# Kernel tuning notes

Measured on AMD Instinct MI355X. Metric: run time of the kernel, lower is better.

## Reference

```python
import jax, jax.numpy as jnp
import numpy as np

INPUT_DIM = 22
H = 256            # lstm_hidden_dim
H1, H2, H3 = 1024, 512, 1024
RRI = 2
N_R = N_L = 2048
N_PAIRS = 65536


def _lstm_layer(x, Wih, Whh, bih, bhh):
    """Bidirectional LSTM layer. x: [T, D]. Wih: [2, 4H, D], Whh: [2, 4H, H],
    bih/bhh: [2, 4H]. PyTorch gate order: i, f, g, o. Returns [T, 2H]."""
    h0 = jnp.zeros((H,), x.dtype)
    c0 = jnp.zeros((H,), x.dtype)

    def run_dir(d, reverse):
        pre = x @ Wih[d].T + (bih[d] + bhh[d])  # [T, 4H] precomputed input part
        Whh_d = Whh[d]

        def step(carry, g_in):
            h, c = carry
            g = g_in + h @ Whh_d.T
            i, f, gg, o = jnp.split(g, 4)
            c = jax.nn.sigmoid(f) * c + jax.nn.sigmoid(i) * jnp.tanh(gg)
            h = jax.nn.sigmoid(o) * jnp.tanh(c)
            return (h, c), h

        _, hs = jax.lax.scan(step, (h0, c0), pre, reverse=reverse)
        return hs  # [T, H], in original time order

    return jnp.concatenate([run_dir(0, False), run_dir(1, True)], axis=-1)


def _encode(x, Wih0, Whh0, bih0, bhh0, Wih1, Whh1, bih1, bhh1,
            W1, b1, W2, b2):
    h = _lstm_layer(x, Wih0, Whh0, bih0, bhh0)      # [T, 2H]
    h = _lstm_layer(h, Wih1, Whh1, bih1, bhh1)      # [T, 2H]
    h = jax.nn.relu(h @ W1.T + b1)                  # [T, H1]
    h = jax.nn.relu(h @ W2.T + b2)                  # [T, H2]
    return h


def setup_inputs() -> dict:
    key = jax.random.key(0)
    ks = jax.random.split(key, 24)
    s = 0.05
    inp = {
        "v_r": jax.random.normal(ks[0], (N_R, INPUT_DIM), jnp.float32),
        "v_l": jax.random.normal(ks[1], (N_L, INPUT_DIM), jnp.float32),
        "pair_r": jax.random.randint(ks[2], (N_PAIRS,), 0, N_R, jnp.int32),
        "pair_l": jax.random.randint(ks[3], (N_PAIRS,), 0, N_L, jnp.int32),
        # LSTM layer 0 (input 22), layer 1 (input 2H); [dir=2, ...]
        "Wih0": jax.random.normal(ks[4], (2, 4 * H, INPUT_DIM), jnp.float32) * s,
        "Whh0": jax.random.normal(ks[5], (2, 4 * H, H), jnp.float32) * s,
        "bih0": jax.random.normal(ks[6], (2, 4 * H), jnp.float32) * s,
        "bhh0": jax.random.normal(ks[7], (2, 4 * H), jnp.float32) * s,
        "Wih1": jax.random.normal(ks[8], (2, 4 * H, 2 * H), jnp.float32) * s,
        "Whh1": jax.random.normal(ks[9], (2, 4 * H, H), jnp.float32) * s,
        "bih1": jax.random.normal(ks[10], (2, 4 * H), jnp.float32) * s,
        "bhh1": jax.random.normal(ks[11], (2, 4 * H), jnp.float32) * s,
        # MLP stacks (PyTorch Linear: y = x W^T + b)
        "W1": jax.random.normal(ks[12], (H1, 2 * H), jnp.float32) * s,
        "b1": jnp.zeros((H1,), jnp.float32),
        "W2": jax.random.normal(ks[13], (H2, H1), jnp.float32) * s,
        "b2": jnp.zeros((H2,), jnp.float32),
        "W3": jax.random.normal(ks[14], (H3, 2 * H2), jnp.float32) * s,
        "b3": jnp.zeros((H3,), jnp.float32),
        "Wout": jax.random.normal(ks[15], (RRI, H3), jnp.float32) * s,
        "bout": jnp.zeros((RRI,), jnp.float32),
    }
    return inp


def reference(v_r, v_l, pair_r, pair_l,
              Wih0, Whh0, bih0, bhh0, Wih1, Whh1, bih1, bhh1,
              W1, b1, W2, b2, W3, b3, Wout, bout):
    # Encode both chains (dropout layers act as identity in eval)
    enc_r = _encode(v_r, Wih0, Whh0, bih0, bhh0, Wih1, Whh1, bih1, bhh1, W1, b1, W2, b2)
    enc_l = _encode(v_l, Wih0, Whh0, bih0, bhh0, Wih1, Whh1, bih1, bhh1, W1, b1, W2, b2)

    # Fused pairwise gather + concat (replaces per-row Python loop)
    w_r = enc_r[pair_r]                      # [P, H2]
    w_l = enc_l[pair_l]                      # [P, H2]
    v_in = jnp.concatenate([w_r, w_l], axis=-1)    # [P, 2*H2]
    v_in_t = jnp.concatenate([w_l, w_r], axis=-1)  # [P, 2*H2]

    h3 = v_in @ W3.T + b3
    h3_t = v_in_t @ W3.T + b3
    out_h3 = jax.nn.relu(0.5 * (h3 + h3_t))        # symmetrized pair rep
    logits = out_h3 @ Wout.T + bout                # [P, rri_size]
    return jax.nn.log_softmax(logits, axis=1)
```

## Files before the change

### kernel.cpp

```cpp
#include <hip/hip_runtime.h>

typedef _Float16 half8 __attribute__((ext_vector_type(8)));
typedef float f32x4 __attribute__((ext_vector_type(4)));

#define AGENT __HIP_MEMORY_SCOPE_AGENT

__device__ __forceinline__ float sigf(float x) { return 1.f / (1.f + __expf(-x)); }
__device__ __forceinline__ float tanhf_(float x) {
  float e = __expf(-2.f * fabsf(x));
  float t = (1.f - e) / (1.f + e);
  return copysignf(t, x);
}

static const size_t O_WGT   = 0;
static const size_t O_XF16  = O_WGT   + (size_t)2*1024*1024;
static const size_t O_WIH0P = O_XF16  + 262144;
static const size_t O_B0P   = O_WIH0P + 131072;
static const size_t O_WIH1P = O_B0P   + 8192;
static const size_t O_B1P   = O_WIH1P + 2097152;
static const size_t O_W1F   = O_B1P   + 8192;
static const size_t O_W2F   = O_W1F   + 1048576;
static const size_t O_W3SF  = O_W2F   + 1048576;
static const size_t O_P0    = O_W3SF  + 1048576;
static const size_t O_H0    = O_P0    + (size_t)32*1024*1024;
static const size_t O_P1    = O_H0    + 4194304;
static const size_t O_H1    = O_P1    + (size_t)32*1024*1024;
static const size_t O_M1    = O_H1    + 4194304;
static const size_t O_E     = O_M1    + 8388608;
static const size_t O_S     = O_E     + 4194304;
static const size_t O_XG    = O_S     + (size_t)16*1024*1024;
static const size_t WS_NEED = O_XG    + 8192;

__global__ void pack_whh(const float* __restrict__ Whh0, const float* __restrict__ Whh1,
                         half8* __restrict__ wgt) {
  int flat = blockIdx.x * 256 + threadIdx.x;
  int lane = flat & 63;
  int kc   = (flat >> 6) & 7;
  int mt   = (flat >> 9) & 63;
  int d    = (flat >> 15) & 1;
  int layer = flat >> 16;
  int m = lane & 15, q = lane >> 4;
  int ul = mt * 4 + (m >> 2), gate = m & 3;
  int grow = gate * 256 + ul;
  const float* src = (layer ? Whh1 : Whh0) + ((size_t)d * 1024 + grow) * 256 + kc * 32 + q * 8;
  half8 v;
#pragma unroll
  for (int j = 0; j < 8; ++j) v[j] = (_Float16)src[j];
  wgt[flat] = v;
}

__global__ void pack_misc(const float* __restrict__ v_r, const float* __restrict__ v_l,
                          const float* __restrict__ Wih0, const float* __restrict__ bih0,
                          const float* __restrict__ bhh0, const float* __restrict__ Wih1,
                          const float* __restrict__ bih1, const float* __restrict__ bhh1,
                          const float* __restrict__ W1, const float* __restrict__ W2,
                          const float* __restrict__ W3,
                          _Float16* __restrict__ xf16, _Float16* __restrict__ wih0p,
                          float* __restrict__ b0p, _Float16* __restrict__ wih1p,
                          float* __restrict__ b1p, _Float16* __restrict__ w1f,
                          _Float16* __restrict__ w2f, _Float16* __restrict__ w3sf) {
  int idx = blockIdx.x * 256 + threadIdx.x;
  if (idx < 131072) {
    int row = idx >> 5, k = idx & 31;
    float v = 0.f;
    if (k < 22) v = (row < 2048) ? v_r[row * 22 + k] : v_l[(row - 2048) * 22 + k];
    xf16[idx] = (_Float16)v;
    return;
  }
  idx -= 131072;
  if (idx < 65536) {
    int d = idx >> 15, jp = (idx >> 5) & 1023, k = idx & 31;
    int u = jp >> 2, g = jp & 3, j = g * 256 + u;
    float v = (k < 22) ? Wih0[((size_t)d * 1024 + j) * 22 + k] : 0.f;
    wih0p[idx] = (_Float16)v;
    return;
  }
  idx -= 65536;
  if (idx < 2048) {
    int d = idx >> 10, jp = idx & 1023;
    int u = jp >> 2, g = jp & 3, j = d * 1024 + g * 256 + u;
    b0p[idx] = bih0[j] + bhh0[j];
    return;
  }
  idx -= 2048;
  if (idx < 1048576) {
    int d = idx >> 19, jp = (idx >> 9) & 1023, k = idx & 511;
    int u = jp >> 2, g = jp & 3;
    wih1p[idx] = (_Float16)Wih1[((size_t)d * 1024 + g * 256 + u) * 512 + k];
    return;
  }
  idx -= 1048576;
  if (idx < 2048) {
    int d = idx >> 10, jp = idx & 1023;
    int u = jp >> 2, g = jp & 3, j = d * 1024 + g * 256 + u;
    b1p[idx] = bih1[j] + bhh1[j];
    return;
  }
  idx -= 2048;
  if (idx < 524288) { w1f[idx] = (_Float16)W1[idx]; return; }
  idx -= 524288;
  if (idx < 524288) { w2f[idx] = (_Float16)W2[idx]; return; }
  idx -= 524288;
  if (idx < 524288) {
    int j = idx >> 9, k = idx & 511;
    w3sf[idx] = (_Float16)(W3[(size_t)j * 1024 + k] + W3[(size_t)j * 1024 + 512 + k]);
    return;
  }
}

__global__ __launch_bounds__(256) void gemm_nt(
    const _Float16* __restrict__ A, const _Float16* __restrict__ B,
    const float* __restrict__ bias, void* __restrict__ Cout,
    int N, int K, int do_relu, int f16out, int hasbias) {
  __shared__ _Float16 as[64][40];
  __shared__ _Float16 bs[64][40];
  const int tid = threadIdx.x;
  const int w = tid >> 6, lane = tid & 63, q = lane >> 4, m15 = lane & 15;
  const int bm = blockIdx.x * 64, bn = blockIdx.y * 64;
  const int srow = tid >> 2, spart = tid & 3;
  f32x4 acc[4] = {};
  for (int k0 = 0; k0 < K; k0 += 32) {
    if (k0) __syncthreads();
    *(half8*)&as[srow][spart * 8] = *(const half8*)(A + (size_t)(bm + srow) * K + k0 + spart * 8);
    *(half8*)&bs[srow][spart * 8] = *(const half8*)(B + (size_t)(bn + srow) * K + k0 + spart * 8);
    __syncthreads();
    half8 af = *(const half8*)&as[w * 16 + m15][q * 8];
#pragma unroll
    for (int ns = 0; ns < 4; ++ns) {
      half8 bf = *(const half8*)&bs[ns * 16 + m15][q * 8];
      acc[ns] = __builtin_amdgcn_mfma_f32_16x16x32_f16(af, bf, acc[ns], 0, 0, 0);
    }
  }
#pragma unroll
  for (int ns = 0; ns < 4; ++ns) {
    int gn = bn + ns * 16 + m15;
    float bv = hasbias ? bias[gn] : 0.f;
#pragma unroll
    for (int r = 0; r < 4; ++r) {
      int gm = bm + w * 16 + q * 4 + r;
      float v = acc[ns][r] + bv;
      if (do_relu) v = fmaxf(v, 0.f);
      if (f16out) ((_Float16*)Cout)[(size_t)gm * N + gn] = (_Float16)v;
      else ((float*)Cout)[(size_t)gm * N + gn] = v;
    }
  }
}

#define MFMAF(Wf, Bf, Acc) __builtin_amdgcn_mfma_f32_16x16x32_f16((Wf), (Bf), (Acc), 0, 0, 0)
__global__ __launch_bounds__(512, 1) void lstm_layer(
    const half8* __restrict__ wgt,
    const float* __restrict__ P,
    _Float16* __restrict__ Hout,
    unsigned* __restrict__ xg,
    int tagbase) {
  __shared__ _Float16 hbuf[2 * 2 * 288];
  __shared__ float4 gbuf[2 * 64];
  const int bid = blockIdx.x;
  const int d = bid >> 2, mq = bid & 3;
  const int tid = threadIdx.x;
  const int w = tid >> 6, lane = tid & 63;
  const int q = lane >> 4, m15 = lane & 15, n2 = m15 & 1;
  const int ug = mq * 64 + lane;
  const int rr = tid - 128;
  const int rp = rr >> 7, ridx = rr & 127;
  const int srcq = (mq + 1 + rp) & 3;
  const int rchain = ridx >> 6, rul = ridx & 63;

  const half8* wb = wgt + ((size_t)((d * 64 + mq * 16 + w * 2) * 8)) * 64 + lane;
#define WLD(ti, kc) wb[((ti) * 8 + (kc)) * 64]
  half8 WA0 = WLD(0, 0), WA1 = WLD(0, 1), WA2 = WLD(0, 2), WA3 = WLD(0, 3);
  half8 WA4 = WLD(0, 4), WA5 = WLD(0, 5), WA6 = WLD(0, 6), WA7 = WLD(0, 7);
  half8 WB0 = WLD(1, 0), WB1 = WLD(1, 1), WB2 = WLD(1, 2), WB3 = WLD(1, 3);
  half8 WB4 = WLD(1, 4), WB5 = WLD(1, 5), WB6 = WLD(1, 6), WB7 = WLD(1, 7);
  for (int i = tid; i < 1152; i += 512) hbuf[i] = (_Float16)0.f;
  float c = 0.f;
  __syncthreads();

  for (int s = 0; s < 2048; ++s) {
    const int t = d ? (2047 - s) : s;
    const int cur = s & 1, nxt = cur ^ 1, par = (s + 1) & 1;
    float4 pv;
    if (w < 2)
      pv = *(const float4*)(P + ((size_t)(d * 4096 + w * 2048 + t)) * 1024 + ug * 4);
    const _Float16* hb = hbuf + (cur * 2 + n2) * 288 + q * 8;
    f32x4 acc0 = {}, acc1 = {};
#define STEPKC(kc) { half8 bf = *(const half8*)(hb + (kc) * 32);  \
    acc0 = MFMAF(WA##kc, bf, acc0); acc1 = MFMAF(WB##kc, bf, acc1); }
    STEPKC(0) STEPKC(1) STEPKC(2) STEPKC(3) STEPKC(4) STEPKC(5) STEPKC(6) STEPKC(7)
    if (m15 < 2) {
      gbuf[m15 * 64 + (w * 2 + 0) * 4 + q] = make_float4(acc0[0], acc0[1], acc0[2], acc0[3]);
      gbuf[m15 * 64 + (w * 2 + 1) * 4 + q] = make_float4(acc1[0], acc1[1], acc1[2], acc1[3]);
    }
    __syncthreads();
    const unsigned tag = (unsigned)(tagbase + s + 1);
    if (w < 2) {
      float4 g = gbuf[w * 64 + lane];
      float xi = g.x + pv.x, xf = g.y + pv.y, xgg = g.z + pv.z, xo = g.w + pv.w;
      float cn = sigf(xf) * c + sigf(xi) * tanhf_(xgg);
      c = cn;
      float h = sigf(xo) * tanhf_(cn);
      _Float16 h16 = (_Float16)h;
      Hout[(size_t)(w * 2048 + t) * 512 + d * 256 + ug] = h16;
      if (s < 2047) {
        hbuf[(nxt * 2 + w) * 288 + ug] = h16;
        unsigned word = (tag << 16) | (unsigned)__builtin_bit_cast(unsigned short, h16);
        __hip_atomic_store(&xg[(((par * 2 + d) * 4 + mq) * 2 + w) * 64 + lane], word,
                           __ATOMIC_RELAXED, AGENT);
      }
    } else if (s < 2047) {
      unsigned* src = &xg[(((par * 2 + d) * 4 + srcq) * 2 + rchain) * 64 + rul];
      unsigned word = __hip_atomic_load(src, __ATOMIC_RELAXED, AGENT);
      while ((word >> 16) != tag) word = __hip_atomic_load(src, __ATOMIC_RELAXED, AGENT);
      hbuf[(nxt * 2 + rchain) * 288 + srcq * 64 + rul] =
          __builtin_bit_cast(_Float16, (unsigned short)(word & 0xffffu));
    }
    __syncthreads();
  }
}

__global__ __launch_bounds__(256) void pair_kernel(
    const float* __restrict__ S, const int* __restrict__ pair_r, const int* __restrict__ pair_l,
    const float* __restrict__ b3, const float* __restrict__ Wout, const float* __restrict__ bout,
    float* __restrict__ out) {
  const int wid = blockIdx.x * 4 + (threadIdx.x >> 6);
  const int lane = threadIdx.x & 63;
  const int r = pair_r[wid], l = pair_l[wid];
  const float* sr = S + (size_t)r * 1024;
  const float* sl = S + (size_t)(2048 + l) * 1024;
  float a0 = 0.f, a1 = 0.f;
#pragma unroll
  for (int cch = 0; cch < 4; ++cch) {
    int j = cch * 256 + lane * 4;
    float4 vr = *(const float4*)(sr + j);
    float4 vl = *(const float4*)(sl + j);
    float4 bb = *(const float4*)(b3 + j);
    float4 w0 = *(const float4*)(Wout + j);
    float4 w1 = *(const float4*)(Wout + 1024 + j);
    float v;
    v = fmaxf(0.f, 0.5f * (vr.x + vl.x) + bb.x); a0 += v * w0.x; a1 += v * w1.x;
    v = fmaxf(0.f, 0.5f * (vr.y + vl.y) + bb.y); a0 += v * w0.y; a1 += v * w1.y;
    v = fmaxf(0.f, 0.5f * (vr.z + vl.z) + bb.z); a0 += v * w0.z; a1 += v * w1.z;
    v = fmaxf(0.f, 0.5f * (vr.w + vl.w) + bb.w); a0 += v * w0.w; a1 += v * w1.w;
  }
#pragma unroll
  for (int off = 32; off; off >>= 1) {
    a0 += __shfl_xor(a0, off, 64);
    a1 += __shfl_xor(a1, off, 64);
  }
  if (lane == 0) {
    float l0 = a0 + bout[0], l1 = a1 + bout[1];
    float m = fmaxf(l0, l1);
    float lse = m + logf(__expf(l0 - m) + __expf(l1 - m));
    out[(size_t)wid * 2] = l0 - lse;
    out[(size_t)wid * 2 + 1] = l1 - lse;
  }
}

extern "C" void kernel_launch(void* const* d_in, const int* in_sizes, int n_in,
                              void* d_out, int out_size, void* d_ws, size_t ws_size,
                              hipStream_t stream) {
  (void)in_sizes; (void)n_in; (void)out_size;
  const float* v_r  = (const float*)d_in[0];
  const float* v_l  = (const float*)d_in[1];
  const int* pair_r = (const int*)d_in[2];
  const int* pair_l = (const int*)d_in[3];
  const float* Wih0 = (const float*)d_in[4];
  const float* Whh0 = (const float*)d_in[5];
  const float* bih0 = (const float*)d_in[6];
  const float* bhh0 = (const float*)d_in[7];
  const float* Wih1 = (const float*)d_in[8];
  const float* Whh1 = (const float*)d_in[9];
  const float* bih1 = (const float*)d_in[10];
  const float* bhh1 = (const float*)d_in[11];
  const float* W1   = (const float*)d_in[12];
  const float* b1   = (const float*)d_in[13];
  const float* W2   = (const float*)d_in[14];
  const float* b2   = (const float*)d_in[15];
  const float* W3   = (const float*)d_in[16];
  const float* b3   = (const float*)d_in[17];
  const float* Wout = (const float*)d_in[18];
  const float* bout = (const float*)d_in[19];

  if (ws_size < WS_NEED) return;
  char* ws = (char*)d_ws;
  half8* wgt      = (half8*)(ws + O_WGT);
  _Float16* xf16  = (_Float16*)(ws + O_XF16);
  _Float16* wih0p = (_Float16*)(ws + O_WIH0P);
  float* b0p      = (float*)(ws + O_B0P);
  _Float16* wih1p = (_Float16*)(ws + O_WIH1P);
  float* b1p      = (float*)(ws + O_B1P);
  _Float16* w1f   = (_Float16*)(ws + O_W1F);
  _Float16* w2f   = (_Float16*)(ws + O_W2F);
  _Float16* w3sf  = (_Float16*)(ws + O_W3SF);
  float* p0       = (float*)(ws + O_P0);
  _Float16* h0    = (_Float16*)(ws + O_H0);
  float* p1       = (float*)(ws + O_P1);
  _Float16* h1    = (_Float16*)(ws + O_H1);
  _Float16* m1    = (_Float16*)(ws + O_M1);
  _Float16* e     = (_Float16*)(ws + O_E);
  float* sbuf     = (float*)(ws + O_S);
  unsigned* xg    = (unsigned*)(ws + O_XG);

  pack_whh<<<512, 256, 0, stream>>>(Whh0, Whh1, wgt);
  pack_misc<<<11024, 256, 0, stream>>>(v_r, v_l, Wih0, bih0, bhh0, Wih1, bih1, bhh1,
                                       W1, W2, W3, xf16, wih0p, b0p, wih1p, b1p, w1f, w2f, w3sf);
  gemm_nt<<<dim3(64, 16), 256, 0, stream>>>(xf16, wih0p, b0p, p0, 1024, 32, 0, 0, 1);
  gemm_nt<<<dim3(64, 16), 256, 0, stream>>>(xf16, wih0p + 32768, b0p + 1024,
                                            p0 + (size_t)4096 * 1024, 1024, 32, 0, 0, 1);
  lstm_layer<<<8, 512, 0, stream>>>(wgt, p0, h0, xg, 4096);
  gemm_nt<<<dim3(64, 16), 256, 0, stream>>>(h0, wih1p, b1p, p1, 1024, 512, 0, 0, 1);
  gemm_nt<<<dim3(64, 16), 256, 0, stream>>>(h0, wih1p + 524288, b1p + 1024,
                                            p1 + (size_t)4096 * 1024, 1024, 512, 0, 0, 1);
  lstm_layer<<<8, 512, 0, stream>>>(wgt + 65536, p1, h1, xg, 8192);
  gemm_nt<<<dim3(64, 16), 256, 0, stream>>>(h1, w1f, b1, m1, 1024, 512, 1, 1, 1);
  gemm_nt<<<dim3(64, 8), 256, 0, stream>>>(m1, w2f, b2, e, 512, 1024, 1, 1, 1);
  gemm_nt<<<dim3(64, 16), 256, 0, stream>>>(e, w3sf, nullptr, sbuf, 1024, 512, 0, 0, 0);
  pair_kernel<<<16384, 256, 0, stream>>>(sbuf, pair_r, pair_l, b3, Wout, bout, (float*)d_out);
}
```

Baseline: 6.297 ms.

## Co-locate LSTM direction blocks per XCD, poll via L2, prefetch next-step gate inputs

The LSTM layer launch grows to 32 blocks, and only blocks with blockIdx%8 in {0,1} do work. This relies on round-robin XCD placement so that the four blocks of one direction share an XCD and its L2, which makes cross-block hidden-state exchange cheaper. Spin-polling now uses an inline-asm sc0 global load that targets L2, with a periodic agent-scope atomic fallback, and the store is also repeated as a volatile write. The precomputed input-gate row for step t+1 is loaded one step ahead to hide global load latency. The scheme depends on undocumented block-to-XCD mapping, and it launches 24 idle blocks.

```diff
diff --git a/kernel.cpp b/kernel.cpp
--- a/kernel.cpp
+++ b/kernel.cpp
@@ -10,6 +10,13 @@
   float e = __expf(-2.f * fabsf(x));
   float t = (1.f - e) / (1.f + e);
   return copysignf(t, x);
+}
+
+__device__ __forceinline__ unsigned poll_l2(const unsigned* p) {
+  unsigned v;
+  asm volatile("global_load_dword %0, %1, off sc0\n\ts_waitcnt vmcnt(0)"
+               : "=v"(v) : "v"(p) : "memory");
+  return v;
 }
 
 static const size_t O_WGT   = 0;
@@ -153,10 +160,11 @@
     _Float16* __restrict__ Hout,
     unsigned* __restrict__ xg,
     int tagbase) {
+  const int xcd = blockIdx.x & 7;
+  if (xcd >= 2) return;
+  const int d = xcd, mq = blockIdx.x >> 3;
   __shared__ _Float16 hbuf[2 * 2 * 288];
   __shared__ float4 gbuf[2 * 64];
-  const int bid = blockIdx.x;
-  const int d = bid >> 2, mq = bid & 3;
   const int tid = threadIdx.x;
   const int w = tid >> 6, lane = tid & 63;
   const int q = lane >> 4, m15 = lane & 15, n2 = m15 & 1;
@@ -174,14 +182,19 @@
   half8 WB4 = WLD(1, 4), WB5 = WLD(1, 5), WB6 = WLD(1, 6), WB7 = WLD(1, 7);
   for (int i = tid; i < 1152; i += 512) hbuf[i] = (_Float16)0.f;
   float c = 0.f;
+  float4 pv;
+  if (w < 2)
+    pv = *(const float4*)(P + ((size_t)(d * 4096 + w * 2048 + (d ? 2047 : 0))) * 1024 + ug * 4);
   __syncthreads();
 
   for (int s = 0; s < 2048; ++s) {
     const int t = d ? (2047 - s) : s;
     const int cur = s & 1, nxt = cur ^ 1, par = (s + 1) & 1;
-    float4 pv;
-    if (w < 2)
-      pv = *(const float4*)(P + ((size_t)(d * 4096 + w * 2048 + t)) * 1024 + ug * 4);
+    float4 pv_next;
+    if (w < 2 && s < 2047) {
+      const int tn = d ? (t - 1) : (t + 1);
+      pv_next = *(const float4*)(P + ((size_t)(d * 4096 + w * 2048 + tn)) * 1024 + ug * 4);
+    }
     const _Float16* hb = hbuf + (cur * 2 + n2) * 288 + q * 8;
     f32x4 acc0 = {}, acc1 = {};
 #define STEPKC(kc) { half8 bf = *(const half8*)(hb + (kc) * 32);  \
@@ -204,16 +217,22 @@
       if (s < 2047) {
         hbuf[(nxt * 2 + w) * 288 + ug] = h16;
         unsigned word = (tag << 16) | (unsigned)__builtin_bit_cast(unsigned short, h16);
-        __hip_atomic_store(&xg[(((par * 2 + d) * 4 + mq) * 2 + w) * 64 + lane], word,
-                           __ATOMIC_RELAXED, AGENT);
+        unsigned* dst = &xg[(((par * 2 + d) * 4 + mq) * 2 + w) * 64 + lane];
+        __hip_atomic_store(dst, word, __ATOMIC_RELAXED, AGENT);
+        *(volatile unsigned*)dst = word;
       }
     } else if (s < 2047) {
-      unsigned* src = &xg[(((par * 2 + d) * 4 + srcq) * 2 + rchain) * 64 + rul];
-      unsigned word = __hip_atomic_load(src, __ATOMIC_RELAXED, AGENT);
-      while ((word >> 16) != tag) word = __hip_atomic_load(src, __ATOMIC_RELAXED, AGENT);
+      const unsigned* src = &xg[(((par * 2 + d) * 4 + srcq) * 2 + rchain) * 64 + rul];
+      unsigned word = poll_l2(src);
+      int k = 0;
+      while ((word >> 16) != tag) {
+        if ((++k & 7) == 0) word = __hip_atomic_load(src, __ATOMIC_RELAXED, AGENT);
+        else word = poll_l2(src);
+      }
       hbuf[(nxt * 2 + rchain) * 288 + srcq * 64 + rul] =
           __builtin_bit_cast(_Float16, (unsigned short)(word & 0xffffu));
     }
+    if (w < 2) pv = pv_next;
     __syncthreads();
   }
 }
@@ -307,11 +326,11 @@
   gemm_nt<<<dim3(64, 16), 256, 0, stream>>>(xf16, wih0p, b0p, p0, 1024, 32, 0, 0, 1);
   gemm_nt<<<dim3(64, 16), 256, 0, stream>>>(xf16, wih0p + 32768, b0p + 1024,
                                             p0 + (size_t)4096 * 1024, 1024, 32, 0, 0, 1);
-  lstm_layer<<<8, 512, 0, stream>>>(wgt, p0, h0, xg, 4096);
+  lstm_layer<<<32, 512, 0, stream>>>(wgt, p0, h0, xg, 4096);
   gemm_nt<<<dim3(64, 16), 256, 0, stream>>>(h0, wih1p, b1p, p1, 1024, 512, 0, 0, 1);
   gemm_nt<<<dim3(64, 16), 256, 0, stream>>>(h0, wih1p + 524288, b1p + 1024,
                                             p1 + (size_t)4096 * 1024, 1024, 512, 0, 0, 1);
-  lstm_layer<<<8, 512, 0, stream>>>(wgt + 65536, p1, h1, xg, 8192);
+  lstm_layer<<<32, 512, 0, stream>>>(wgt + 65536, p1, h1, xg, 8192);
   gemm_nt<<<dim3(64, 16), 256, 0, stream>>>(h1, w1f, b1, m1, 1024, 512, 1, 1, 1);
   gemm_nt<<<dim3(64, 8), 256, 0, stream>>>(m1, w2f, b2, e, 512, 1024, 1, 1, 1);
   gemm_nt<<<dim3(64, 16), 256, 0, stream>>>(e, w3sf, nullptr, sbuf, 1024, 512, 0, 0, 0);
```

New measurement: 6.904 ms. +9.6%, slower.

## Split each LSTM direction across two blocks and prefetch next-step input gates

Applied to the files above, without the earlier changes.

Each recurrent LSTM direction now runs on 2 workgroups instead of 4. Each workgroup holds twice as many Whh tiles in registers (four accumulators per wave) and exchanges hidden state with a single peer instead of three, which cuts the cross-block spin-wait traffic per timestep. The precomputed input-gate values for the next timestep are also loaded one step ahead so their global-memory latency overlaps the MFMA work. In exchange, each block does twice the per-step matrix work and uses more registers.

```diff
diff --git a/kernel.cpp b/kernel.cpp
--- a/kernel.cpp
+++ b/kernel.cpp
@@ -153,67 +153,78 @@
     _Float16* __restrict__ Hout,
     unsigned* __restrict__ xg,
     int tagbase) {
+  const int d = blockIdx.x >> 1, mh = blockIdx.x & 1;
   __shared__ _Float16 hbuf[2 * 2 * 288];
-  __shared__ float4 gbuf[2 * 64];
-  const int bid = blockIdx.x;
-  const int d = bid >> 2, mq = bid & 3;
+  __shared__ float4 gbuf[2 * 128];
   const int tid = threadIdx.x;
   const int w = tid >> 6, lane = tid & 63;
   const int q = lane >> 4, m15 = lane & 15, n2 = m15 & 1;
-  const int ug = mq * 64 + lane;
-  const int rr = tid - 128;
-  const int rp = rr >> 7, ridx = rr & 127;
-  const int srcq = (mq + 1 + rp) & 3;
-  const int rchain = ridx >> 6, rul = ridx & 63;
-
-  const half8* wb = wgt + ((size_t)((d * 64 + mq * 16 + w * 2) * 8)) * 64 + lane;
+  const int uchain = (tid >> 7) & 1, ul = tid & 127;
+  const int ug = mh * 128 + ul;
+  const int rr = tid - 256;
+  const int rchain = (rr >> 7) & 1, rul = rr & 127;
+
+  const half8* wb = wgt + ((size_t)((d * 64 + mh * 32 + w * 4) * 8)) * 64 + lane;
 #define WLD(ti, kc) wb[((ti) * 8 + (kc)) * 64]
   half8 WA0 = WLD(0, 0), WA1 = WLD(0, 1), WA2 = WLD(0, 2), WA3 = WLD(0, 3);
   half8 WA4 = WLD(0, 4), WA5 = WLD(0, 5), WA6 = WLD(0, 6), WA7 = WLD(0, 7);
   half8 WB0 = WLD(1, 0), WB1 = WLD(1, 1), WB2 = WLD(1, 2), WB3 = WLD(1, 3);
   half8 WB4 = WLD(1, 4), WB5 = WLD(1, 5), WB6 = WLD(1, 6), WB7 = WLD(1, 7);
+  half8 WC0 = WLD(2, 0), WC1 = WLD(2, 1), WC2 = WLD(2, 2), WC3 = WLD(2, 3);
+  half8 WC4 = WLD(2, 4), WC5 = WLD(2, 5), WC6 = WLD(2, 6), WC7 = WLD(2, 7);
+  half8 WD0 = WLD(3, 0), WD1 = WLD(3, 1), WD2 = WLD(3, 2), WD3 = WLD(3, 3);
+  half8 WD4 = WLD(3, 4), WD5 = WLD(3, 5), WD6 = WLD(3, 6), WD7 = WLD(3, 7);
   for (int i = tid; i < 1152; i += 512) hbuf[i] = (_Float16)0.f;
   float c = 0.f;
+  float4 pv;
+  if (w < 4)
+    pv = *(const float4*)(P + ((size_t)(d * 4096 + uchain * 2048 + (d ? 2047 : 0))) * 1024 + ug * 4);
   __syncthreads();
 
   for (int s = 0; s < 2048; ++s) {
     const int t = d ? (2047 - s) : s;
     const int cur = s & 1, nxt = cur ^ 1, par = (s + 1) & 1;
-    float4 pv;
-    if (w < 2)
-      pv = *(const float4*)(P + ((size_t)(d * 4096 + w * 2048 + t)) * 1024 + ug * 4);
+    float4 pv_next;
+    if (w < 4 && s < 2047) {
+      const int tn = d ? (t - 1) : (t + 1);
+      pv_next = *(const float4*)(P + ((size_t)(d * 4096 + uchain * 2048 + tn)) * 1024 + ug * 4);
+    }
     const _Float16* hb = hbuf + (cur * 2 + n2) * 288 + q * 8;
-    f32x4 acc0 = {}, acc1 = {};
+    f32x4 acc0 = {}, acc1 = {}, acc2 = {}, acc3 = {};
 #define STEPKC(kc) { half8 bf = *(const half8*)(hb + (kc) * 32);  \
-    acc0 = MFMAF(WA##kc, bf, acc0); acc1 = MFMAF(WB##kc, bf, acc1); }
+    acc0 = MFMAF(WA##kc, bf, acc0); acc1 = MFMAF(WB##kc, bf, acc1); \
+    acc2 = MFMAF(WC##kc, bf, acc2); acc3 = MFMAF(WD##kc, bf, acc3); }
     STEPKC(0) STEPKC(1) STEPKC(2) STEPKC(3) STEPKC(4) STEPKC(5) STEPKC(6) STEPKC(7)
     if (m15 < 2) {
-      gbuf[m15 * 64 + (w * 2 + 0) * 4 + q] = make_float4(acc0[0], acc0[1], acc0[2], acc0[3]);
-      gbuf[m15 * 64 + (w * 2 + 1) * 4 + q] = make_float4(acc1[0], acc1[1], acc1[2], acc1[3]);
+      gbuf[m15 * 128 + (w * 4 + 0) * 4 + q] = make_float4(acc0[0], acc0[1], acc0[2], acc0[3]);
+      gbuf[m15 * 128 + (w * 4 + 1) * 4 + q] = make_float4(acc1[0], acc1[1], acc1[2], acc1[3]);
+      gbuf[m15 * 128 + (w * 4 + 2) * 4 + q] = make_float4(acc2[0], acc2[1], acc2[2], acc2[3]);
+      gbuf[m15 * 128 + (w * 4 + 3) * 4 + q] = make_float4(acc3[0], acc3[1], acc3[2], acc3[3]);
     }
     __syncthreads();
     const unsigned tag = (unsigned)(tagbase + s + 1);
-    if (w < 2) {
-      float4 g = gbuf[w * 64 + lane];
+    if (w < 4) {
+      float4 g = gbuf[uchain * 128 + ul];
       float xi = g.x + pv.x, xf = g.y + pv.y, xgg = g.z + pv.z, xo = g.w + pv.w;
       float cn = sigf(xf) * c + sigf(xi) * tanhf_(xgg);
       c = cn;
       float h = sigf(xo) * tanhf_(cn);
       _Float16 h16 = (_Float16)h;
-      Hout[(size_t)(w * 2048 + t) * 512 + d * 256 + ug] = h16;
+      Hout[(size_t)(uchain * 2048 + t) * 512 + d * 256 + ug] = h16;
       if (s < 2047) {
-        hbuf[(nxt * 2 + w) * 288 + ug] = h16;
+        hbuf[(nxt * 2 + uchain) * 288 + ug] = h16;
         unsigned word = (tag << 16) | (unsigned)__builtin_bit_cast(unsigned short, h16);
-        __hip_atomic_store(&xg[(((par * 2 + d) * 4 + mq) * 2 + w) * 64 + lane], word,
+        __hip_atomic_store(&xg[((par * 2 + d) * 2 + mh) * 256 + tid], word,
                            __ATOMIC_RELAXED, AGENT);
       }
     } else if (s < 2047) {
-      unsigned* src = &xg[(((par * 2 + d) * 4 + srcq) * 2 + rchain) * 64 + rul];
+      unsigned* src = &xg[((par * 2 + d) * 2 + (1 - mh)) * 256 + rr];
       unsigned word = __hip_atomic_load(src, __ATOMIC_RELAXED, AGENT);
       while ((word >> 16) != tag) word = __hip_atomic_load(src, __ATOMIC_RELAXED, AGENT);
-      hbuf[(nxt * 2 + rchain) * 288 + srcq * 64 + rul] =
+      hbuf[(nxt * 2 + rchain) * 288 + (1 - mh) * 128 + rul] =
           __builtin_bit_cast(_Float16, (unsigned short)(word & 0xffffu));
     }
+    if (w < 4) pv = pv_next;
     __syncthreads();
   }
 }
@@ -307,11 +318,11 @@
   gemm_nt<<<dim3(64, 16), 256, 0, stream>>>(xf16, wih0p, b0p, p0, 1024, 32, 0, 0, 1);
   gemm_nt<<<dim3(64, 16), 256, 0, stream>>>(xf16, wih0p + 32768, b0p + 1024,
                                             p0 + (size_t)4096 * 1024, 1024, 32, 0, 0, 1);
-  lstm_layer<<<8, 512, 0, stream>>>(wgt, p0, h0, xg, 4096);
+  lstm_layer<<<4, 512, 0, stream>>>(wgt, p0, h0, xg, 4096);
   gemm_nt<<<dim3(64, 16), 256, 0, stream>>>(h0, wih1p, b1p, p1, 1024, 512, 0, 0, 1);
   gemm_nt<<<dim3(64, 16), 256, 0, stream>>>(h0, wih1p + 524288, b1p + 1024,
                                             p1 + (size_t)4096 * 1024, 1024, 512, 0, 0, 1);
-  lstm_layer<<<8, 512, 0, stream>>>(wgt + 65536, p1, h1, xg, 8192);
+  lstm_layer<<<4, 512, 0, stream>>>(wgt + 65536, p1, h1, xg, 8192);
   gemm_nt<<<dim3(64, 16), 256, 0, stream>>>(h1, w1f, b1, m1, 1024, 512, 1, 1, 1);
   gemm_nt<<<dim3(64, 8), 256, 0, stream>>>(m1, w2f, b2, e, 512, 1024, 1, 1, 1);
   gemm_nt<<<dim3(64, 16), 256, 0, stream>>>(e, w3sf, nullptr, sbuf, 1024, 512, 0, 0, 0);
```

Result: slower. 7.390 ms (+17.4%).
